# Performance work log

Hardware: AMD Instinct MI355X
Metric: run time of the kernel (lower is better)

Reference implementation:

```python
import jax, jax.numpy as jnp
import numpy as np

B, S, Dm, H, W, G = 2, 4096, 768, 12, 256, 16
HD = Dm // H
NEG = -10000.0


def _band_qk(q, k, w):
    # q,k: [B,S,H,D] -> banded scores [B,S,H,2w+1]; slot j = key position i-w+j
    Bq, Sq, Hq, Dq = q.shape
    nb = Sq // w
    qb = q.reshape(Bq, nb, w, Hq, Dq)
    kp = jnp.pad(k, ((0, 0), (w, w), (0, 0), (0, 0)))
    idx = (jnp.arange(nb) * w)[:, None] + jnp.arange(3 * w)[None, :]
    kb = kp[:, idx]                                    # [B,nb,3w,H,D]
    s = jnp.einsum('btxhd,btyhd->bthxy', qb, kb)       # [B,nb,H,w,3w]
    r = jnp.arange(w)[:, None]
    c = r + jnp.arange(2 * w + 1)[None, :]
    band = s[..., r, c]                                # [B,nb,H,w,2w+1]
    return band.transpose(0, 1, 3, 2, 4).reshape(Bq, Sq, Hq, 2 * w + 1)


def _band_pv(p, v, w):
    # p: [B,S,H,2w+1], v: [B,S,H,D] -> [B,S,H,D]
    Bp, Sp, Hp, _ = p.shape
    Dv = v.shape[-1]
    nb = Sp // w
    vp = jnp.pad(v, ((0, 0), (w, w), (0, 0), (0, 0)))
    idx = (jnp.arange(nb) * w)[:, None] + jnp.arange(3 * w)[None, :]
    vb = vp[:, idx]                                    # [B,nb,3w,H,D]
    pb = p.reshape(Bp, nb, w, Hp, 2 * w + 1).transpose(0, 1, 3, 2, 4)
    r = jnp.arange(w)[:, None]
    c = r + jnp.arange(2 * w + 1)[None, :]
    pband = jnp.zeros((Bp, nb, Hp, w, 3 * w), p.dtype).at[..., r, c].set(pb)
    out = jnp.einsum('bthxy,btyhd->btxhd', pband, vb)  # [B,nb,w,H,D]
    return out.reshape(Bp, Sp, Hp, Dv)


def setup_inputs() -> dict:
    key = jax.random.key(0)
    ks = jax.random.split(key, 13)
    inp = {'hidden_states': jax.random.normal(ks[0], (B, S, Dm), dtype=jnp.float32)}
    names = ['Wq', 'bq', 'Wk', 'bk', 'Wv', 'bv', 'Wqg', 'bqg', 'Wkg', 'bkg', 'Wvg', 'bvg']
    for i, n in enumerate(names):
        sh = (Dm, Dm) if n.startswith('W') else (Dm,)
        inp[n] = 0.02 * jax.random.normal(ks[i + 1], sh, dtype=jnp.float32)
    inp['n_global'] = G
    return inp


def reference(hidden_states, Wq, bq, Wk, bk, Wv, bv, Wqg, bqg, Wkg, bkg, Wvg, bvg, n_global):
    Bh, Sh, D = hidden_states.shape
    hd = D // H
    w, g = W, n_global
    scale = 1.0 / jnp.sqrt(jnp.float32(hd))
    q = ((hidden_states @ Wq + bq) * scale).reshape(Bh, Sh, H, hd)
    k = (hidden_states @ Wk + bk).reshape(Bh, Sh, H, hd)
    v = (hidden_states @ Wv + bv).reshape(Bh, Sh, H, hd)
    # banded local attention scores (mask_invalid_locations -> -inf outside seq)
    band = _band_qk(q, k, w)                           # [B,S,H,2w+1]
    i = jnp.arange(Sh)[:, None]
    j = jnp.arange(2 * w + 1)[None, :]
    kpos = i - w + j                                   # key position per window slot
    valid = (kpos >= 0) & (kpos < Sh)
    band = jnp.where(valid[None, :, None, :], band, -jnp.inf)
    # remove global keys from windowed attention (-10000 float mask)
    band = band + jnp.where(valid & (kpos < g), NEG, 0.0)[None, :, None, :]
    # global columns: every query attends to global keys (local k projection)
    sel = jnp.einsum('bihd,bghd->bihg', q, k[:, :g])
    logits = jnp.concatenate([sel, band], axis=-1)     # [B,S,H,g+2w+1]
    probs = jax.nn.softmax(logits.astype(jnp.float32), axis=-1)
    attn = jnp.einsum('bihg,bghd->bihd', probs[..., :g], v[:, :g])
    attn = attn + _band_pv(probs[..., g:], v, w)       # [B,S,H,hd]
    # global token rows: full attention with global projections
    qg = ((hidden_states[:, :g] @ Wqg + bqg) * scale).reshape(Bh, g, H, hd)
    kg = (hidden_states @ Wkg + bkg).reshape(Bh, Sh, H, hd)
    vg = (hidden_states @ Wvg + bvg).reshape(Bh, Sh, H, hd)
    gl = jnp.einsum('bghd,bshd->bhgs', qg, kg)
    gp = jax.nn.softmax(gl.astype(jnp.float32), axis=-1)
    out_g = jnp.einsum('bhgs,bshd->bghd', gp, vg)      # [B,g,H,hd]
    attn = attn.at[:, :g].set(out_g)
    return attn.reshape(Bh, Sh, D)
```

## Files before the change

kernel.cpp:

```cpp
#include <hip/hip_runtime.h>

constexpr int Bc = 2, Sc = 4096, Dmc = 768, Hc = 12, HDc = 64, Wc = 256, Gc = 16;
constexpr int NCH = 16, CHK = 256;
constexpr float LOG2E = 1.4426950408889634f;
constexpr float SCALE2q = 0.125f * LOG2E;
constexpr float NEG2c = -10000.0f * LOG2E;

typedef __attribute__((ext_vector_type(8))) short s16x8;
typedef __attribute__((ext_vector_type(4))) short s16x4;
typedef __attribute__((ext_vector_type(4))) float f32x4;
typedef __attribute__((ext_vector_type(2))) unsigned int u32x2;

#define DEVINL __device__ __forceinline__

DEVINL float b2f(short x) {
  unsigned int u = ((unsigned int)(unsigned short)x) << 16;
  return __builtin_bit_cast(float, u);
}
DEVINL short f2b(float f) {
  unsigned int u = __builtin_bit_cast(unsigned int, f);
  unsigned int r = (u + 0x7fffu + ((u >> 16) & 1u)) >> 16;
  return (short)r;
}
DEVINL void gload16(const short* g, const short* l) {
  __builtin_amdgcn_global_load_lds(
      (const __attribute__((address_space(1))) void*)g,
      (__attribute__((address_space(3))) void*)l, 16, 0, 0);
}
DEVINL float max3f(float a, float b, float c) { return fmaxf(fmaxf(a, b), c); }

__global__ __launch_bounds__(256) void conv_bf16(
    const float* __restrict__ src, short* __restrict__ dst)
{
  const size_t i = ((size_t)blockIdx.x * 256 + threadIdx.x) * 8;
  f32x4 a = *(const f32x4*)(src + i);
  f32x4 c = *(const f32x4*)(src + i + 4);
  s16x8 r;
#pragma unroll
  for (int u = 0; u < 4; ++u) { r[u] = f2b(a[u]); r[4 + u] = f2b(c[u]); }
  *(s16x8*)(dst + i) = r;
}

__global__ __launch_bounds__(256) void transpose_w(
    const float* __restrict__ W0, const float* __restrict__ W1, const float* __restrict__ W2,
    short* __restrict__ T0, short* __restrict__ T1, short* __restrict__ T2)
{
  const float* W = blockIdx.z == 0 ? W0 : (blockIdx.z == 1 ? W1 : W2);
  short* T = blockIdx.z == 0 ? T0 : (blockIdx.z == 1 ? T1 : T2);
  __shared__ short t[32][33];
  const int k0 = blockIdx.x * 32, n0 = blockIdx.y * 32;
  const int a = threadIdx.x >> 3, cg = (threadIdx.x & 7) * 4;
  f32x4 v = *(const f32x4*)&W[(size_t)(k0 + a) * Dmc + n0 + cg];
#pragma unroll
  for (int u = 0; u < 4; ++u) t[a][cg + u] = f2b(v[u]);
  __syncthreads();
  s16x4 s;
#pragma unroll
  for (int u = 0; u < 4; ++u) s[u] = t[cg + u][a];
  *(s16x4*)&T[(size_t)(n0 + a) * Dmc + k0 + cg] = s;
}

__global__ __launch_bounds__(256) void gemm_fused(
    const short* __restrict__ X, const short* __restrict__ Wt,
    const float* __restrict__ b0, const float* __restrict__ b1, const float* __restrict__ b2,
    short* __restrict__ Y0, float scale0)
{
  __shared__ short lds[16384];
  char* ldsb = (char*)lds;
  const int tid = threadIdx.x, lane = tid & 63, wid = tid >> 6;
  const int gy = gridDim.y;

  const int rawd = blockIdx.x + 64 * blockIdx.y;
  const int wgid = (rawd & 7) * (gy * 8) + (rawd >> 3);
  const int mi0 = wgid / gy, ny = wgid - mi0 * gy;
  const int m0 = mi0 * 128;
  const int nch = ny / 6, ncol = (ny % 6) * 128;
  const int n0g = ny * 128;

  short* Y = Y0 + (size_t)nch * 6291456;
  const float* bias = nch == 0 ? b0 : (nch == 1 ? b1 : b2);
  const float scale = nch == 0 ? scale0 : 1.0f;

  const int lr = lane & 15, lq = lane >> 4;
  const int wm = (wid & 1) * 64, wn = (wid >> 1) * 64;

  const int l8 = lane >> 3, l7 = lane & 7;
  const int colsh = ((l7 * 16) ^ (l8 << 4)) >> 1;
  const short* Aptr[4];
  const short* Bptr[4];
#pragma unroll
  for (int i = 0; i < 4; ++i) {
    Aptr[i] = X  + (size_t)(m0  + wid * 32 + i * 8 + l8) * Dmc + colsh;
    Bptr[i] = Wt + (size_t)(n0g + wid * 32 + i * 8 + l8) * Dmc + colsh;
  }

  int arb[4][2], brb[4][2];
#pragma unroll
  for (int mi = 0; mi < 4; ++mi)
#pragma unroll
    for (int ks = 0; ks < 2; ++ks) {
      int row = wm + mi * 16 + lr;
      arb[mi][ks] = row * 128 + ((lq * 16 + ks * 64) ^ ((row & 7) << 4));
    }
#pragma unroll
  for (int ni = 0; ni < 4; ++ni)
#pragma unroll
    for (int ks = 0; ks < 2; ++ks) {
      int row = wn + ni * 16 + lr;
      brb[ni][ks] = 16384 + row * 128 + ((lq * 16 + ks * 64) ^ ((row & 7) << 4));
    }

  f32x4 acc[4][4] = {};

  for (int kt = 0; kt < 12; ++kt) {
    const int ko = kt * 64;
    if (kt) __syncthreads();
#pragma unroll
    for (int i = 0; i < 4; ++i) {
      gload16(Aptr[i] + ko, &lds[wid * 2048 + i * 512]);
      gload16(Bptr[i] + ko, &lds[8192 + wid * 2048 + i * 512]);
    }
    asm volatile("s_waitcnt vmcnt(0)" ::: "memory");
    __syncthreads();
#pragma unroll
    for (int ks = 0; ks < 2; ++ks) {
      s16x8 af[4], bf[4];
#pragma unroll
      for (int mi = 0; mi < 4; ++mi) af[mi] = *(const s16x8*)(ldsb + arb[mi][ks]);
#pragma unroll
      for (int ni = 0; ni < 4; ++ni) bf[ni] = *(const s16x8*)(ldsb + brb[ni][ks]);
#pragma unroll
      for (int mi = 0; mi < 4; ++mi)
#pragma unroll
        for (int ni = 0; ni < 4; ++ni)
          acc[mi][ni] = __builtin_amdgcn_mfma_f32_16x16x32_bf16(af[mi], bf[ni], acc[mi][ni], 0, 0, 0);
    }
  }

#pragma unroll
  for (int mi = 0; mi < 4; ++mi)
#pragma unroll
    for (int ni = 0; ni < 4; ++ni) {
      int col = ncol + wn + ni * 16 + lr;
      float bv_ = bias[col];
#pragma unroll
      for (int r = 0; r < 4; ++r) {
        int row = m0 + wm + mi * 16 + lq * 4 + r;
        Y[(size_t)row * Dmc + col] = f2b((acc[mi][ni][r] + bv_) * scale);
      }
    }
}

__global__ __launch_bounds__(256) void qg_proj(
    const float* __restrict__ hs, const float* __restrict__ Wqg,
    const float* __restrict__ bqg, float* __restrict__ qg)
{
  const int row = blockIdx.x;
  const int b = row / Gc, i = row % Gc;
  const int tid = threadIdx.x;
  const int n = blockIdx.y * 128 + (tid & 127);
  const int half = tid >> 7;
  __shared__ float x[Dmc];
  __shared__ float part[128];
  for (int c = tid; c < Dmc; c += 256)
    x[c] = b2f(f2b(hs[((size_t)(b * Sc + i)) * Dmc + c]));
  __syncthreads();
  float acc = 0.f;
#pragma unroll 4
  for (int c = half * 384; c < half * 384 + 384; ++c)
    acc = fmaf(x[c], b2f(f2b(Wqg[(size_t)c * Dmc + n])), acc);
  if (half) part[tid & 127] = acc;
  __syncthreads();
  if (!half)
    qg[(size_t)row * Dmc + n] = (acc + part[tid] + bqg[n]) * SCALE2q;
}

__global__ __launch_bounds__(256) void local_attn_mfma(
    const short* __restrict__ q, const short* __restrict__ k,
    const short* __restrict__ v, float* __restrict__ out)
{
  const int raw = blockIdx.x + 64 * (blockIdx.y + 12 * blockIdx.z);
  const int swz = (raw & 7) * 192 + (raw >> 3);
  const int q0 = (swz & 63) * 64;
  const int h = (swz >> 6) % 12, b = swz / 768;
  const int tid = threadIdx.x, lane = tid & 63, wid = tid >> 6;

  __shared__ short Ks[4096];
  __shared__ short Vt[4096];
  __shared__ short Ps[4][1024];
  char* KsB = (char*)Ks;
  char* VtB = (char*)Vt;

  const int ql = lane & 15;
  const int lg = lane >> 4;
  const int qr = wid * 16 + ql;

  s16x8 qf[2];
  {
    const short* qp = q + ((size_t)(b * Sc + q0 + qr)) * Dmc + h * HDc + lg * 8;
    qf[0] = *(const s16x8*)qp;
    qf[1] = *(const s16x8*)(qp + 32);
  }

  f32x4 oacc[4] = {};
  float m_run = -INFINITY, l_run = 0.f;

  const int krow = tid >> 3, kcol16 = (tid & 7) * 16;
  const int vp = tid & 31, vo = tid >> 5;
  const size_t hoff = (size_t)h * HDc;
  const size_t brow = (size_t)b * Sc;

  const bool interior = (q0 >= 256) && (q0 <= Sc - 384);

  auto keyof = [&](int c) {
    int key = (c < Gc) ? c : q0 - 272 + c;
    return min(max(key, 0), Sc - 1);
  };

  const short *kp0, *kp1, *vp0, *vp1;
  s16x8 kreg0, kreg1, vreg0, vreg1;
  auto loadRegs = [&](int ch) {
    if (!interior || ch <= 1) {
      kp0 = k + (brow + keyof(ch * 64 + krow))       * Dmc + hoff + (kcol16 >> 1);
      kp1 = k + (brow + keyof(ch * 64 + 32 + krow))  * Dmc + hoff + (kcol16 >> 1);
      vp0 = v + (brow + keyof(ch * 64 + 2 * vp))      * Dmc + hoff + vo * 8;
      vp1 = v + (brow + keyof(ch * 64 + 2 * vp + 1))  * Dmc + hoff + vo * 8;
    } else {
      kp0 += 64 * Dmc; kp1 += 64 * Dmc; vp0 += 64 * Dmc; vp1 += 64 * Dmc;
    }
    kreg0 = *(const s16x8*)kp0;
    kreg1 = *(const s16x8*)kp1;
    vreg0 = *(const s16x8*)vp0;
    vreg1 = *(const s16x8*)vp1;
  };

  loadRegs(0);

  for (int ch = 0; ch < 10; ++ch) {
    __syncthreads();
    *(s16x8*)(KsB + krow * 128        + (kcol16 ^ ((krow & 7) << 4))) = kreg0;
    *(s16x8*)(KsB + (krow + 32) * 128 + (kcol16 ^ ((krow & 7) << 4))) = kreg1;
#pragma unroll
    for (int j = 0; j < 8; ++j) {
      int d = vo * 8 + j;
      unsigned int wrd = (unsigned int)(unsigned short)vreg0[j] |
                         ((unsigned int)(unsigned short)vreg1[j] << 16);
      *(unsigned int*)(VtB + d * 128 + ((4 * vp) ^ (j << 4))) = wrd;
    }
    if (ch < 9) loadRegs(ch + 1);
    __syncthreads();

    if (ch == 9 && wid != 3) continue;

    f32x4 sac[4] = {};
    __builtin_amdgcn_s_setprio(1);
#pragma unroll
    for (int kt = 0; kt < 4; ++kt) {
      int row = kt * 16 + ql;
#pragma unroll
      for (int sl = 0; sl < 2; ++sl) {
        s16x8 af = *(const s16x8*)(KsB + row * 128 + ((lg * 16 + sl * 64) ^ ((row & 7) << 4)));
        sac[kt] = __builtin_amdgcn_mfma_f32_16x16x32_bf16(af, qf[sl], sac[kt], 0, 0, 0);
      }
    }
    __builtin_amdgcn_s_setprio(0);

    bool needMask = (ch < 2) | (ch > 7) | (q0 < 272) | (q0 > Sc - 384);
    if (needMask) {
#pragma unroll
      for (int kt = 0; kt < 4; ++kt)
#pragma unroll
        for (int r = 0; r < 4; ++r) {
          int c = ch * 64 + kt * 16 + lg * 4 + r;
          if (c >= Gc) {
            float sv = sac[kt][r];
            int jj = c - Gc - qr;
            int kp2 = q0 - 272 + c;
            bool ok = (jj >= 0) & (jj <= 2 * Wc) & (kp2 >= 0) & (kp2 < Sc);
            sac[kt][r] = ok ? (sv + ((kp2 < Gc) ? NEG2c : 0.f)) : -INFINITY;
          }
        }
    }

    float t0 = max3f(sac[0][0], sac[0][1], sac[0][2]);
    float t1 = max3f(sac[0][3], sac[1][0], sac[1][1]);
    float t2 = max3f(sac[1][2], sac[1][3], sac[2][0]);
    float t3 = max3f(sac[2][1], sac[2][2], sac[2][3]);
    float t4 = max3f(sac[3][0], sac[3][1], sac[3][2]);
    float cm = fmaxf(max3f(t0, t1, t2), max3f(t3, t4, sac[3][3]));
    cm = fmaxf(cm, __shfl_xor(cm, 16));
    cm = fmaxf(cm, __shfl_xor(cm, 32));

    if (__all(cm <= m_run + 11.5f)) {
      float cl0 = 0.f, cl1 = 0.f, cl2 = 0.f, cl3 = 0.f;
#pragma unroll
      for (int kt = 0; kt < 4; ++kt) {
        float p0 = __builtin_amdgcn_exp2f(sac[kt][0] - m_run);
        float p1 = __builtin_amdgcn_exp2f(sac[kt][1] - m_run);
        float p2 = __builtin_amdgcn_exp2f(sac[kt][2] - m_run);
        float p3 = __builtin_amdgcn_exp2f(sac[kt][3] - m_run);
        sac[kt][0] = p0; sac[kt][1] = p1; sac[kt][2] = p2; sac[kt][3] = p3;
        cl0 += p0; cl1 += p1; cl2 += p2; cl3 += p3;
      }
      float cl = (cl0 + cl1) + (cl2 + cl3);
      cl += __shfl_xor(cl, 16);
      cl += __shfl_xor(cl, 32);
      l_run += cl;
    } else {
      float m_new = fmaxf(m_run, cm);
      float scale = __builtin_amdgcn_exp2f(m_run - m_new);
      float cl0 = 0.f, cl1 = 0.f, cl2 = 0.f, cl3 = 0.f;
#pragma unroll
      for (int kt = 0; kt < 4; ++kt) {
        float p0 = __builtin_amdgcn_exp2f(sac[kt][0] - m_new);
        float p1 = __builtin_amdgcn_exp2f(sac[kt][1] - m_new);
        float p2 = __builtin_amdgcn_exp2f(sac[kt][2] - m_new);
        float p3 = __builtin_amdgcn_exp2f(sac[kt][3] - m_new);
        sac[kt][0] = p0; sac[kt][1] = p1; sac[kt][2] = p2; sac[kt][3] = p3;
        cl0 += p0; cl1 += p1; cl2 += p2; cl3 += p3;
      }
      float cl = (cl0 + cl1) + (cl2 + cl3);
      cl += __shfl_xor(cl, 16);
      cl += __shfl_xor(cl, 32);
      l_run = l_run * scale + cl;
      m_run = m_new;
#pragma unroll
      for (int rr = 0; rr < 4; ++rr) {
        float os = __shfl(scale, lg * 4 + rr);
#pragma unroll
        for (int dt = 0; dt < 4; ++dt) oacc[dt][rr] *= os;
      }
    }

    char* PsB = (char*)Ps[wid];
#pragma unroll
    for (int kt = 0; kt < 4; ++kt) {
      u32x2 pw;
      asm("v_cvt_pk_bf16_f32 %0, %1, %2" : "=v"(pw.x) : "v"(sac[kt][0]), "v"(sac[kt][1]));
      asm("v_cvt_pk_bf16_f32 %0, %1, %2" : "=v"(pw.y) : "v"(sac[kt][2]), "v"(sac[kt][3]));
      *(u32x2*)(PsB + ql * 128 + ((kt * 32 + lg * 8) ^ ((ql & 7) << 4))) = pw;
    }
    s16x8 pf[2];
#pragma unroll
    for (int ks = 0; ks < 2; ++ks)
      pf[ks] = *(const s16x8*)(PsB + ql * 128 + ((ks * 64 + lg * 16) ^ ((ql & 7) << 4)));
    __builtin_amdgcn_s_setprio(1);
#pragma unroll
    for (int dt = 0; dt < 4; ++dt) {
      int d = dt * 16 + ql;
#pragma unroll
      for (int ks = 0; ks < 2; ++ks) {
        s16x8 vf = *(const s16x8*)(VtB + d * 128 + ((ks * 64 + lg * 16) ^ ((d & 7) << 4)));
        oacc[dt] = __builtin_amdgcn_mfma_f32_16x16x32_bf16(pf[ks], vf, oacc[dt], 0, 0, 0);
      }
    }
    __builtin_amdgcn_s_setprio(0);
  }

  float inv = 1.f / l_run;
#pragma unroll
  for (int rr = 0; rr < 4; ++rr) {
    float oi = __shfl(inv, lg * 4 + rr);
    int row = q0 + wid * 16 + lg * 4 + rr;
    float* op = out + ((size_t)(b * Sc + row)) * Dmc + h * HDc + ql;
#pragma unroll
    for (int dt = 0; dt < 4; ++dt)
      op[dt * 16] = oacc[dt][rr] * oi;
  }
}

__global__ __launch_bounds__(256) void global_attn_part(
    const float* __restrict__ qg, const short* __restrict__ kg,
    const short* __restrict__ vg, float* __restrict__ pml, float* __restrict__ po)
{
  const int ch = blockIdx.x & (NCH - 1);
  const int i  = blockIdx.x >> 4;
  const int h = blockIdx.y, b = blockIdx.z;
  const int tid = threadIdx.x, lane = tid & 63, wid = tid >> 6;

  __shared__ float qrow[64];
  __shared__ float pls[CHK];
  __shared__ float red[8];
  __shared__ float osum[4][64];

  if (tid < 64) qrow[tid] = qg[(size_t)(b * Gc + i) * Dmc + h * HDc + tid];
  __syncthreads();

  const int sk = ch * CHK + tid;
  const s16x8* kr = (const s16x8*)(kg + ((size_t)(b * Sc + sk)) * Dmc + h * HDc);
  float acc = 0.f;
#pragma unroll
  for (int c = 0; c < 8; ++c) {
    s16x8 kv = kr[c];
#pragma unroll
    for (int u = 0; u < 8; ++u) acc = fmaf(qrow[c * 8 + u], b2f(kv[u]), acc);
  }

  float m = acc;
#pragma unroll
  for (int off = 32; off > 0; off >>= 1) m = fmaxf(m, __shfl_xor(m, off));
  if (lane == 0) red[wid] = m;
  __syncthreads();
  m = fmaxf(fmaxf(red[0], red[1]), fmaxf(red[2], red[3]));

  float p = __builtin_amdgcn_exp2f(acc - m);
  pls[tid] = p;
  float ls = p;
#pragma unroll
  for (int off = 32; off > 0; off >>= 1) ls += __shfl_xor(ls, off);
  if (lane == 0) red[4 + wid] = ls;
  __syncthreads();
  const float l = red[4] + red[5] + red[6] + red[7];

  const int jg = tid >> 3, db = (tid & 7) * 8;
  float o[8] = {};
  const short* vb2 = vg + ((size_t)(b * Sc + ch * CHK + jg * 8)) * Dmc + h * HDc + db;
#pragma unroll
  for (int jj = 0; jj < 8; ++jj) {
    float pw = pls[jg * 8 + jj];
    s16x8 vv = *(const s16x8*)(vb2 + (size_t)jj * Dmc);
#pragma unroll
    for (int u = 0; u < 8; ++u) o[u] = fmaf(pw, b2f(vv[u]), o[u]);
  }
#pragma unroll
  for (int mk = 8; mk <= 32; mk <<= 1)
#pragma unroll
    for (int u = 0; u < 8; ++u) o[u] += __shfl_xor(o[u], mk);
  if ((lane & 56) == 0) {
#pragma unroll
    for (int u = 0; u < 8; ++u) osum[wid][(lane & 7) * 8 + u] = o[u];
  }
  __syncthreads();

  const size_t slot = (((size_t)(b * Hc + h) * Gc + i) * NCH + ch);
  if (tid < 64)
    po[slot * 64 + tid] = osum[0][tid] + osum[1][tid] + osum[2][tid] + osum[3][tid];
  if (tid == 0) { pml[slot * 2] = m; pml[slot * 2 + 1] = l; }
}

__global__ __launch_bounds__(64) void global_attn_comb(
    const float* __restrict__ pml, const float* __restrict__ po,
    float* __restrict__ out)
{
  const int i = blockIdx.x, h = blockIdx.y, b = blockIdx.z;
  const int d = threadIdx.x;
  const size_t base = ((size_t)(b * Hc + h) * Gc + i) * NCH;

  float m = -INFINITY;
#pragma unroll
  for (int ch = 0; ch < NCH; ++ch) m = fmaxf(m, pml[(base + ch) * 2]);
  float l = 0.f, o = 0.f;
#pragma unroll
  for (int ch = 0; ch < NCH; ++ch) {
    float wgt = __builtin_amdgcn_exp2f(pml[(base + ch) * 2] - m);
    l = fmaf(pml[(base + ch) * 2 + 1], wgt, l);
    o = fmaf(po[(base + ch) * 64 + d], wgt, o);
  }
  out[((size_t)(b * Sc + i)) * Dmc + h * HDc + d] = o / l;
}

extern "C" void kernel_launch(void* const* d_in, const int* in_sizes, int n_in,
                              void* d_out, int out_size, void* d_ws, size_t ws_size,
                              hipStream_t stream) {
  const float* hs  = (const float*)d_in[0];
  const float* Wq  = (const float*)d_in[1];
  const float* bq  = (const float*)d_in[2];
  const float* Wk  = (const float*)d_in[3];
  const float* bk  = (const float*)d_in[4];
  const float* Wv  = (const float*)d_in[5];
  const float* bv  = (const float*)d_in[6];
  const float* Wqg = (const float*)d_in[7];
  const float* bqg = (const float*)d_in[8];
  const float* Wkg = (const float*)d_in[9];
  const float* bkg = (const float*)d_in[10];
  const float* Wvg = (const float*)d_in[11];
  const float* bvg = (const float*)d_in[12];
  float* out = (float*)d_out;

  char* ws = (char*)d_ws;
  const size_t bufB = (size_t)Bc * Sc * Dmc * sizeof(short);
  short* hsb = (short*)(ws);
  short* s1  = (short*)(ws + bufB);
  short* s2  = (short*)(ws + 2 * bufB);
  short* s3  = (short*)(ws + 3 * bufB);

  short* wtA = (short*)d_out;
  short* wtB = wtA + (size_t)Dmc * Dmc;
  short* wtC = wtB + (size_t)Dmc * Dmc;
  float* qg  = (float*)(ws + 3 * bufB);
  float* pml = (float*)(ws + 3 * bufB + 98304);
  float* po  = (float*)(ws + 3 * bufB + 147456);
  short* wtD = (short*)(ws + 3 * bufB + (4u << 20));
  short* wtE = wtD + (size_t)Dmc * Dmc;

  dim3 bb(256);
  conv_bf16<<<dim3(3072), bb, 0, stream>>>(hs, hsb);
  transpose_w<<<dim3(24, 24, 3), bb, 0, stream>>>(Wq, Wk, Wv, wtA, wtB, wtC);

  gemm_fused<<<dim3(64, 18), bb, 0, stream>>>(hsb, wtA, bq, bk, bv, s1, SCALE2q);

  local_attn_mfma<<<dim3(64, Hc, Bc), bb, 0, stream>>>(s1, s2, s3, out);

  transpose_w<<<dim3(24, 24, 2), bb, 0, stream>>>(Wkg, Wvg, Wvg, wtD, wtE, wtE);
  gemm_fused<<<dim3(64, 12), bb, 0, stream>>>(hsb, wtD, bkg, bvg, bvg, s1, 1.0f);

  qg_proj<<<dim3(Bc * Gc, Dmc / 128), bb, 0, stream>>>(hs, Wqg, bqg, qg);
  global_attn_part<<<dim3(Gc * NCH, Hc, Bc), bb, 0, stream>>>(qg, s1, s2, pml, po);
  global_attn_comb<<<dim3(Gc, Hc, Bc), dim3(64), 0, stream>>>(pml, po, out);
}
```

Measured before the change: 189.5 us.

## Rewrite global-token attention partials with MFMA over all 16 queries per chunk

The global attention partial kernel switches from one 256-thread block per (query, 256-key chunk) doing scalar FMAs to one 64-lane wave per 64-key chunk. Each wave handles all 16 global queries together using bf16 MFMA for both QK and PV, and stages K and transposed V in swizzled LDS. qg is now stored as bf16, and the combine kernel merges 64 chunk partials laid out per query row. This removes redundant K/V reads, since each key is now loaded once for all 16 queries instead of 16 times. The cost is lower precision for qg and P, plus a longer combine loop.

```diff
diff --git a/kernel.cpp b/kernel.cpp
--- a/kernel.cpp
+++ b/kernel.cpp
@@ -1,7 +1,7 @@
 #include <hip/hip_runtime.h>
 
 constexpr int Bc = 2, Sc = 4096, Dmc = 768, Hc = 12, HDc = 64, Wc = 256, Gc = 16;
-constexpr int NCH = 16, CHK = 256;
+constexpr int NCHG = 64;
 constexpr float LOG2E = 1.4426950408889634f;
 constexpr float SCALE2q = 0.125f * LOG2E;
 constexpr float NEG2c = -10000.0f * LOG2E;
@@ -153,7 +153,7 @@
 
 __global__ __launch_bounds__(256) void qg_proj(
     const float* __restrict__ hs, const float* __restrict__ Wqg,
-    const float* __restrict__ bqg, float* __restrict__ qg)
+    const float* __restrict__ bqg, short* __restrict__ qg)
 {
   const int row = blockIdx.x;
   const int b = row / Gc, i = row % Gc;
@@ -172,7 +172,7 @@
   if (half) part[tid & 127] = acc;
   __syncthreads();
   if (!half)
-    qg[(size_t)row * Dmc + n] = (acc + part[tid] + bqg[n]) * SCALE2q;
+    qg[(size_t)row * Dmc + n] = f2b((acc + part[tid] + bqg[n]) * SCALE2q);
 }
 
 __global__ __launch_bounds__(256) void local_attn_mfma(
@@ -369,73 +369,123 @@
   }
 }
 
-__global__ __launch_bounds__(256) void global_attn_part(
-    const float* __restrict__ qg, const short* __restrict__ kg,
+__global__ __launch_bounds__(64) void global_attn_part_mfma(
+    const short* __restrict__ qg, const short* __restrict__ kg,
     const short* __restrict__ vg, float* __restrict__ pml, float* __restrict__ po)
 {
-  const int ch = blockIdx.x & (NCH - 1);
-  const int i  = blockIdx.x >> 4;
-  const int h = blockIdx.y, b = blockIdx.z;
-  const int tid = threadIdx.x, lane = tid & 63, wid = tid >> 6;
-
-  __shared__ float qrow[64];
-  __shared__ float pls[CHK];
-  __shared__ float red[8];
-  __shared__ float osum[4][64];
-
-  if (tid < 64) qrow[tid] = qg[(size_t)(b * Gc + i) * Dmc + h * HDc + tid];
-  __syncthreads();
-
-  const int sk = ch * CHK + tid;
-  const s16x8* kr = (const s16x8*)(kg + ((size_t)(b * Sc + sk)) * Dmc + h * HDc);
-  float acc = 0.f;
-#pragma unroll
-  for (int c = 0; c < 8; ++c) {
-    s16x8 kv = kr[c];
-#pragma unroll
-    for (int u = 0; u < 8; ++u) acc = fmaf(qrow[c * 8 + u], b2f(kv[u]), acc);
-  }
-
-  float m = acc;
-#pragma unroll
-  for (int off = 32; off > 0; off >>= 1) m = fmaxf(m, __shfl_xor(m, off));
-  if (lane == 0) red[wid] = m;
-  __syncthreads();
-  m = fmaxf(fmaxf(red[0], red[1]), fmaxf(red[2], red[3]));
-
-  float p = __builtin_amdgcn_exp2f(acc - m);
-  pls[tid] = p;
-  float ls = p;
-#pragma unroll
-  for (int off = 32; off > 0; off >>= 1) ls += __shfl_xor(ls, off);
-  if (lane == 0) red[4 + wid] = ls;
-  __syncthreads();
-  const float l = red[4] + red[5] + red[6] + red[7];
-
-  const int jg = tid >> 3, db = (tid & 7) * 8;
-  float o[8] = {};
-  const short* vb2 = vg + ((size_t)(b * Sc + ch * CHK + jg * 8)) * Dmc + h * HDc + db;
-#pragma unroll
-  for (int jj = 0; jj < 8; ++jj) {
-    float pw = pls[jg * 8 + jj];
-    s16x8 vv = *(const s16x8*)(vb2 + (size_t)jj * Dmc);
-#pragma unroll
-    for (int u = 0; u < 8; ++u) o[u] = fmaf(pw, b2f(vv[u]), o[u]);
-  }
-#pragma unroll
-  for (int mk = 8; mk <= 32; mk <<= 1)
-#pragma unroll
-    for (int u = 0; u < 8; ++u) o[u] += __shfl_xor(o[u], mk);
-  if ((lane & 56) == 0) {
-#pragma unroll
-    for (int u = 0; u < 8; ++u) osum[wid][(lane & 7) * 8 + u] = o[u];
-  }
-  __syncthreads();
-
-  const size_t slot = (((size_t)(b * Hc + h) * Gc + i) * NCH + ch);
-  if (tid < 64)
-    po[slot * 64 + tid] = osum[0][tid] + osum[1][tid] + osum[2][tid] + osum[3][tid];
-  if (tid == 0) { pml[slot * 2] = m; pml[slot * 2 + 1] = l; }
+  const int ch = blockIdx.x, h = blockIdx.y, b = blockIdx.z;
+  const int lane = threadIdx.x;
+
+  __shared__ short Ks[4096];
+  __shared__ short Vt[4096];
+  __shared__ short Ps[1024];
+  char* KsB = (char*)Ks;
+  char* VtB = (char*)Vt;
+
+  const int ql = lane & 15;
+  const int lg = lane >> 4;
+
+  s16x8 qf[2];
+  {
+    const short* qp = qg + ((size_t)(b * Gc + ql)) * Dmc + h * HDc + lg * 8;
+    qf[0] = *(const s16x8*)qp;
+    qf[1] = *(const s16x8*)(qp + 32);
+  }
+
+  const size_t hoff = (size_t)h * HDc;
+  const size_t brow = (size_t)b * Sc;
+  const int key0 = ch * 64;
+
+  const int krow = lane >> 3, kcol16 = (lane & 7) * 16;
+#pragma unroll
+  for (int rr = 0; rr < 8; ++rr) {
+    int row = krow + rr * 8;
+    s16x8 kv = *(const s16x8*)(kg + (brow + key0 + row) * Dmc + hoff + (kcol16 >> 1));
+    *(s16x8*)(KsB + row * 128 + (kcol16 ^ ((row & 7) << 4))) = kv;
+  }
+  const int vp = lane & 31, vo0 = lane >> 5;
+#pragma unroll
+  for (int oo = 0; oo < 4; ++oo) {
+    int vo = vo0 + oo * 2;
+    s16x8 v0 = *(const s16x8*)(vg + (brow + key0 + 2 * vp)     * Dmc + hoff + vo * 8);
+    s16x8 v1 = *(const s16x8*)(vg + (brow + key0 + 2 * vp + 1) * Dmc + hoff + vo * 8);
+#pragma unroll
+    for (int j = 0; j < 8; ++j) {
+      int d = vo * 8 + j;
+      unsigned int wrd = (unsigned int)(unsigned short)v0[j] |
+                         ((unsigned int)(unsigned short)v1[j] << 16);
+      *(unsigned int*)(VtB + d * 128 + ((4 * vp) ^ (j << 4))) = wrd;
+    }
+  }
+
+  f32x4 sac[4] = {};
+#pragma unroll
+  for (int kt = 0; kt < 4; ++kt) {
+    int row = kt * 16 + ql;
+#pragma unroll
+    for (int sl = 0; sl < 2; ++sl) {
+      s16x8 af = *(const s16x8*)(KsB + row * 128 + ((lg * 16 + sl * 64) ^ ((row & 7) << 4)));
+      sac[kt] = __builtin_amdgcn_mfma_f32_16x16x32_bf16(af, qf[sl], sac[kt], 0, 0, 0);
+    }
+  }
+
+  float t0 = max3f(sac[0][0], sac[0][1], sac[0][2]);
+  float t1 = max3f(sac[0][3], sac[1][0], sac[1][1]);
+  float t2 = max3f(sac[1][2], sac[1][3], sac[2][0]);
+  float t3 = max3f(sac[2][1], sac[2][2], sac[2][3]);
+  float t4 = max3f(sac[3][0], sac[3][1], sac[3][2]);
+  float m = fmaxf(max3f(t0, t1, t2), max3f(t3, t4, sac[3][3]));
+  m = fmaxf(m, __shfl_xor(m, 16));
+  m = fmaxf(m, __shfl_xor(m, 32));
+
+  float cl = 0.f;
+#pragma unroll
+  for (int kt = 0; kt < 4; ++kt)
+#pragma unroll
+    for (int r = 0; r < 4; ++r) {
+      float p = __builtin_amdgcn_exp2f(sac[kt][r] - m);
+      sac[kt][r] = p;
+      cl += p;
+    }
+  cl += __shfl_xor(cl, 16);
+  cl += __shfl_xor(cl, 32);
+
+#pragma unroll
+  for (int kt = 0; kt < 4; ++kt) {
+    u32x2 pw;
+    asm("v_cvt_pk_bf16_f32 %0, %1, %2" : "=v"(pw.x) : "v"(sac[kt][0]), "v"(sac[kt][1]));
+    asm("v_cvt_pk_bf16_f32 %0, %1, %2" : "=v"(pw.y) : "v"(sac[kt][2]), "v"(sac[kt][3]));
+    *(u32x2*)((char*)Ps + ql * 128 + ((kt * 32 + lg * 8) ^ ((ql & 7) << 4))) = pw;
+  }
+  s16x8 pf[2];
+#pragma unroll
+  for (int ks = 0; ks < 2; ++ks)
+    pf[ks] = *(const s16x8*)((char*)Ps + ql * 128 + ((ks * 64 + lg * 16) ^ ((ql & 7) << 4)));
+
+  f32x4 oacc[4] = {};
+#pragma unroll
+  for (int dt = 0; dt < 4; ++dt) {
+    int d = dt * 16 + ql;
+#pragma unroll
+    for (int ks = 0; ks < 2; ++ks) {
+      s16x8 vf = *(const s16x8*)(VtB + d * 128 + ((ks * 64 + lg * 16) ^ ((d & 7) << 4)));
+      oacc[dt] = __builtin_amdgcn_mfma_f32_16x16x32_bf16(pf[ks], vf, oacc[dt], 0, 0, 0);
+    }
+  }
+
+  const size_t slot = ((size_t)(b * Hc + h) * NCHG + ch);
+  float* pob = po + slot * 1024;
+#pragma unroll
+  for (int rr = 0; rr < 4; ++rr) {
+    int qrow = lg * 4 + rr;
+#pragma unroll
+    for (int dt = 0; dt < 4; ++dt)
+      pob[qrow * 64 + dt * 16 + ql] = oacc[dt][rr];
+  }
+  if (lg == 0) {
+    pml[(slot * 16 + ql) * 2]     = m;
+    pml[(slot * 16 + ql) * 2 + 1] = cl;
+  }
 }
 
 __global__ __launch_bounds__(64) void global_attn_comb(
@@ -444,17 +494,17 @@
 {
   const int i = blockIdx.x, h = blockIdx.y, b = blockIdx.z;
   const int d = threadIdx.x;
-  const size_t base = ((size_t)(b * Hc + h) * Gc + i) * NCH;
+  const size_t base = (size_t)(b * Hc + h) * NCHG;
 
   float m = -INFINITY;
-#pragma unroll
-  for (int ch = 0; ch < NCH; ++ch) m = fmaxf(m, pml[(base + ch) * 2]);
+#pragma unroll 8
+  for (int ch = 0; ch < NCHG; ++ch) m = fmaxf(m, pml[((base + ch) * 16 + i) * 2]);
   float l = 0.f, o = 0.f;
-#pragma unroll
-  for (int ch = 0; ch < NCH; ++ch) {
-    float wgt = __builtin_amdgcn_exp2f(pml[(base + ch) * 2] - m);
-    l = fmaf(pml[(base + ch) * 2 + 1], wgt, l);
-    o = fmaf(po[(base + ch) * 64 + d], wgt, o);
+#pragma unroll 8
+  for (int ch = 0; ch < NCHG; ++ch) {
+    float wgt = __builtin_amdgcn_exp2f(pml[((base + ch) * 16 + i) * 2] - m);
+    l = fmaf(pml[((base + ch) * 16 + i) * 2 + 1], wgt, l);
+    o = fmaf(po[(base + ch) * 1024 + i * 64 + d], wgt, o);
   }
   out[((size_t)(b * Sc + i)) * Dmc + h * HDc + d] = o / l;
 }
@@ -487,10 +537,10 @@
   short* wtA = (short*)d_out;
   short* wtB = wtA + (size_t)Dmc * Dmc;
   short* wtC = wtB + (size_t)Dmc * Dmc;
-  float* qg  = (float*)(ws + 3 * bufB);
-  float* pml = (float*)(ws + 3 * bufB + 98304);
-  float* po  = (float*)(ws + 3 * bufB + 147456);
-  short* wtD = (short*)(ws + 3 * bufB + (4u << 20));
+  short* qgb = (short*)(ws + 3 * bufB);
+  float* pml = (float*)(ws + 3 * bufB + 65536);
+  float* po  = (float*)(ws + 3 * bufB + (1u << 20));
+  short* wtD = (short*)(ws + 3 * bufB + (8u << 20));
   short* wtE = wtD + (size_t)Dmc * Dmc;
 
   dim3 bb(256);
@@ -504,7 +554,7 @@
   transpose_w<<<dim3(24, 24, 2), bb, 0, stream>>>(Wkg, Wvg, Wvg, wtD, wtE, wtE);
   gemm_fused<<<dim3(64, 12), bb, 0, stream>>>(hsb, wtD, bkg, bvg, bvg, s1, 1.0f);
 
-  qg_proj<<<dim3(Bc * Gc, Dmc / 128), bb, 0, stream>>>(hs, Wqg, bqg, qg);
-  global_attn_part<<<dim3(Gc * NCH, Hc, Bc), bb, 0, stream>>>(qg, s1, s2, pml, po);
+  qg_proj<<<dim3(Bc * Gc, Dmc / 128), bb, 0, stream>>>(hs, Wqg, bqg, qgb);
+  global_attn_part_mfma<<<dim3(NCHG, Hc, Bc), dim3(64), 0, stream>>>(qgb, s1, s2, pml, po);
   global_attn_comb<<<dim3(Gc, Hc, Bc), dim3(64), 0, stream>>>(pml, po, out);
 }
```

New measurement: 176.9 us. -6.6%, faster.
